# Kernel tuning notes

Hardware: AMD Instinct MI355X
Metric: run time of the kernel (lower is better)

The kernel has to match this reference:

```python
import jax, jax.numpy as jnp
import numpy as np

B, NQ, NK, D_IN, HD = 1, 16384, 7933, 1024, 512
R = 0.3  # keep-top-r fraction used for the quantile threshold


def _l2norm(x):
    # matches F.normalize(p=2, dim=-1, eps=1e-12)
    n = jnp.linalg.norm(x, axis=-1, keepdims=True)
    return x / jnp.maximum(n, 1e-12)


def setup_inputs() -> dict:
    key = jax.random.key(0)
    ks = jax.random.split(key, 10)
    s = 0.02
    return {
        "query": jax.random.normal(ks[0], (B, NQ, D_IN), jnp.float32),
        "key_x": jax.random.normal(ks[1], (B, NK, D_IN), jnp.float32),
        "wq_w": jax.random.normal(ks[2], (HD, D_IN), jnp.float32) * s,
        "wq_b": jnp.zeros((HD,), jnp.float32),
        "wk_w": jax.random.normal(ks[3], (HD, D_IN), jnp.float32) * s,
        "wk_b": jnp.zeros((HD,), jnp.float32),
        "wa_w": jax.random.normal(ks[4], (1, NK), jnp.float32) * s,
        "wa_b": jnp.zeros((1,), jnp.float32),
        "cls_w": jax.random.normal(ks[5], (1, HD), jnp.float32) * s,
        "cls_b": jnp.zeros((1,), jnp.float32),
    }


def reference(query, key_x, wq_w, wq_b, wk_w, wk_b, wa_w, wa_b, cls_w, cls_b):
    # WQ / WK: Linear + Tanh
    q = jnp.tanh(jnp.einsum("bnd,hd->bnh", query, wq_w) + wq_b)   # [B,NQ,HD]
    k = jnp.tanh(jnp.einsum("bnd,hd->bnh", key_x, wk_w) + wk_b)   # [B,NK,HD]
    # normalized dot-product scores
    A = jnp.einsum("bqh,bkh->bqk", _l2norm(q), _l2norm(k))        # [B,NQ,NK]
    # WA: Linear(NK -> 1)
    A1 = jnp.einsum("bqk,ok->bqo", A, wa_w) + wa_b                # [B,NQ,1]
    # quantile threshold from batch 0 (torch: sorted ascending, index -int(r*NQ))
    thre = jax.lax.stop_gradient(jnp.sort(A1[0, :, 0])[-int(R * NQ)])
    A1 = jnp.where(A1 > thre, A1, 0.0)                            # F.threshold(., thre, 0)
    attn = jax.nn.softmax(A1, axis=1)                             # softmax over NQ (zeros included)
    attn_t = jnp.transpose(attn, (0, 2, 1))                       # [B,1,NQ]
    z = jnp.matmul(attn_t, q).reshape(-1, HD)                     # [B,HD]
    y_prob = z @ cls_w.T + cls_b                                  # [B,1]
    return (y_prob, attn_t)
```

## Files before the change

### kernel.cpp

```cpp
#include <hip/hip_runtime.h>
#include <math.h>

#define NQ 16384
#define NK 7933
#define DI 1024
#define HD 512
#define RANK_TARGET 11469

typedef __bf16 bf16x8 __attribute__((ext_vector_type(8)));
typedef float  f32x4  __attribute__((ext_vector_type(4)));

#define GLOAD_LDS16(g, l)                                                     \
  __builtin_amdgcn_global_load_lds(                                           \
      (const __attribute__((address_space(1))) void*)(g),                     \
      (__attribute__((address_space(3))) void*)(l), 16, 0, 0)

__device__ __forceinline__ unsigned mapf(float f) {
  unsigned b = __float_as_uint(f);
  return (b & 0x80000000u) ? ~b : (b | 0x80000000u);
}

__global__ void conv_all(const float* __restrict__ q, const float* __restrict__ k,
                         const float* __restrict__ wq, const float* __restrict__ wk,
                         __bf16* __restrict__ qbf, __bf16* __restrict__ kbf,
                         __bf16* __restrict__ wqbf, __bf16* __restrict__ wkbf,
                         unsigned* __restrict__ zero_region) {
  if (blockIdx.x == 0) {
    for (int j = threadIdx.x; j < 1088; j += 256) zero_region[j] = 0u;
  }
  const int NQ8 = NQ * DI / 8;
  const int NK8 = NK * DI / 8;
  const int W8  = HD * DI / 8;
  const int total = NQ8 + NK8 + 2 * W8;
  int i = blockIdx.x * blockDim.x + threadIdx.x;
  int stride = gridDim.x * blockDim.x;
  for (; i < total; i += stride) {
    const float* s; __bf16* d; int j;
    if (i < NQ8)                 { s = q;  d = qbf;  j = i; }
    else if (i < NQ8 + NK8)      { s = k;  d = kbf;  j = i - NQ8; }
    else if (i < NQ8 + NK8 + W8) { s = wq; d = wqbf; j = i - NQ8 - NK8; }
    else                         { s = wk; d = wkbf; j = i - NQ8 - NK8 - W8; }
    float4 a = ((const float4*)s)[2 * j];
    float4 b = ((const float4*)s)[2 * j + 1];
    bf16x8 o;
    o[0] = (__bf16)a.x; o[1] = (__bf16)a.y; o[2] = (__bf16)a.z; o[3] = (__bf16)a.w;
    o[4] = (__bf16)b.x; o[5] = (__bf16)b.y; o[6] = (__bf16)b.z; o[7] = (__bf16)b.w;
    ((bf16x8*)d)[j] = o;
  }
}

template <bool FUSE_A1>
__global__ __launch_bounds__(256, 3)
void gemm_bt_tanh(const __bf16* __restrict__ A, const __bf16* __restrict__ B,
                  const float* __restrict__ bias, float* __restrict__ C, int M,
                  const float* __restrict__ v, float* __restrict__ A1dot,
                  float* __restrict__ A1ss) {
  constexpr int K = DI;
  constexpr int N = HD;
  __shared__ __align__(16) __bf16 sA[128 * 64];
  __shared__ __align__(16) __bf16 sB[128 * 64];

  const int tid  = threadIdx.x;
  const int lane = tid & 63;
  const int wave = tid >> 6;
  const int wr = wave >> 1, wc = wave & 1;
  const int m0 = blockIdx.x * 128, n0 = blockIdx.y * 128;

  const int srow = lane >> 3;
  const int scol = (((lane & 7) ^ srow)) << 3;

  const int lrow = lane & 15;
  const int chi  = lane >> 4;

  f32x4 acc[4][4] = {};

  for (int kk = 0; kk < K; kk += 64) {
    __syncthreads();
#pragma unroll
    for (int c = 0; c < 4; ++c) {
      int seg = wave * 4 + c;
      int row = seg * 8 + srow;
      int ga = m0 + row; if (ga > M - 1) ga = M - 1;
      GLOAD_LDS16(A + (size_t)ga * K + kk + scol, &sA[seg * 512]);
      GLOAD_LDS16(B + (size_t)(n0 + row) * K + kk + scol, &sB[seg * 512]);
    }
    __syncthreads();
#pragma unroll
    for (int ks = 0; ks < 64; ks += 32) {
      const int cc = (ks >> 3) + chi;
      const int sw = ((cc ^ (lrow & 7)) << 3);
      bf16x8 af[4], bfr[4];
#pragma unroll
      for (int mi = 0; mi < 4; ++mi)
        af[mi] = *(const bf16x8*)(&sA[(wr * 64 + mi * 16 + lrow) * 64 + sw]);
#pragma unroll
      for (int ni = 0; ni < 4; ++ni)
        bfr[ni] = *(const bf16x8*)(&sB[(wc * 64 + ni * 16 + lrow) * 64 + sw]);
#pragma unroll
      for (int mi = 0; mi < 4; ++mi)
#pragma unroll
        for (int ni = 0; ni < 4; ++ni)
          acc[mi][ni] = __builtin_amdgcn_mfma_f32_16x16x32_bf16(af[mi], bfr[ni], acc[mi][ni], 0, 0, 0);
    }
  }

  const int rbase = m0 + wr * 64 + ((lane >> 4) << 2);
  const int cbase = n0 + wc * 64 + (lane & 15);
  float b4[4], v4[4];
#pragma unroll
  for (int ni = 0; ni < 4; ++ni) {
    b4[ni] = bias[cbase + ni * 16];
    if constexpr (FUSE_A1) v4[ni] = v[cbase + ni * 16];
  }
#pragma unroll
  for (int mi = 0; mi < 4; ++mi) {
#pragma unroll
    for (int r = 0; r < 4; ++r) {
      int grow = rbase + mi * 16 + r;
      if (grow < M) {
        float pd = 0.f, pss = 0.f;
#pragma unroll
        for (int ni = 0; ni < 4; ++ni) {
          float val = tanhf(acc[mi][ni][r] + b4[ni]);
          C[(size_t)grow * N + cbase + ni * 16] = val;
          if constexpr (FUSE_A1) { pd += val * v4[ni]; pss += val * val; }
        }
        if constexpr (FUSE_A1) {
#pragma unroll
          for (int off = 1; off < 16; off <<= 1) {
            pd += __shfl_xor(pd, off);
            pss += __shfl_xor(pss, off);
          }
          if ((lane & 15) == 0) {
            atomicAdd(&A1dot[grow], pd);
            atomicAdd(&A1ss[grow], pss);
          }
        }
      }
    }
  }
}

__global__ __launch_bounds__(256)
void reduce_v_zero(const float* __restrict__ kt, const float* __restrict__ wa,
                   float* __restrict__ v, int M, uint2* __restrict__ zr) {
  {
    int g = blockIdx.x * 256 + threadIdx.x;
    uint2 zz; zz.x = 0u; zz.y = 0u;
    zr[g] = zz;
    if (g < 24576 - 16384) zr[16384 + g] = zz;
  }
  __shared__ float vpart[4][512];
  const int tid = threadIdx.x, lane = tid & 63, wave = tid >> 6;
  const int gw = blockIdx.x * 4 + wave;
  const int tw = gridDim.x * 4;
  float acc[8] = {0, 0, 0, 0, 0, 0, 0, 0};
  for (int r = gw; r < M; r += tw) {
    const float4* p = (const float4*)(kt + (size_t)r * HD + lane * 8);
    float4 x = p[0], y = p[1];
    float ss = x.x * x.x + x.y * x.y + x.z * x.z + x.w * x.w
             + y.x * y.x + y.y * y.y + y.z * y.z + y.w * y.w;
#pragma unroll
    for (int off = 32; off; off >>= 1) ss += __shfl_xor(ss, off);
    float s = wa[r] / fmaxf(sqrtf(ss), 1e-12f);
    acc[0] += s * x.x; acc[1] += s * x.y; acc[2] += s * x.z; acc[3] += s * x.w;
    acc[4] += s * y.x; acc[5] += s * y.y; acc[6] += s * y.z; acc[7] += s * y.w;
  }
#pragma unroll
  for (int j = 0; j < 8; ++j) vpart[wave][lane * 8 + j] = acc[j];
  __syncthreads();
  for (int c = tid; c < 512; c += 256)
    atomicAdd(&v[c], vpart[0][c] + vpart[1][c] + vpart[2][c] + vpart[3][c]);
}

__global__ __launch_bounds__(1024)
void select_kernel(const float* __restrict__ A1dot, const float* __restrict__ A1ss,
                   const float* __restrict__ wa_b, float* __restrict__ A1,
                   unsigned* __restrict__ keyg, float* __restrict__ scf) {
  __shared__ unsigned wred1[16], wred2[16], wred3[16];
  __shared__ unsigned s_res;
  const int t = threadIdx.x, lane = t & 63, wave = t >> 6;
  const float wab = wa_b[0];
  unsigned kloc[16];
#pragma unroll 4
  for (int j = 0; j < 16; ++j) {
    int i = j * 1024 + t;
    float d = A1dot[i], ss = A1ss[i];
    float a1 = d / fmaxf(sqrtf(ss), 1e-12f) + wab;
    A1[i] = a1;
    unsigned k = mapf(a1);
    kloc[j] = k;
    keyg[i] = k;
  }
  if (t == 0) s_res = 0u;
  __syncthreads();

  for (int b = 30; b >= 0; b -= 2) {
    const unsigned res = s_res;
    const unsigned t1 = res | (1u << b);
    const unsigned t2 = res | (2u << b);
    const unsigned t3 = res | (3u << b);
    unsigned c1 = 0, c2 = 0, c3 = 0;
#pragma unroll
    for (int j = 0; j < 16; ++j) {
      unsigned k = kloc[j];
      c1 += (k < t1); c2 += (k < t2); c3 += (k < t3);
    }
#pragma unroll
    for (int off = 32; off; off >>= 1) {
      c1 += __shfl_xor(c1, off);
      c2 += __shfl_xor(c2, off);
      c3 += __shfl_xor(c3, off);
    }
    if (lane == 0) { wred1[wave] = c1; wred2[wave] = c2; wred3[wave] = c3; }
    __syncthreads();
    if (t == 0) {
      unsigned C1 = 0, C2 = 0, C3 = 0;
      for (int w = 0; w < 16; ++w) { C1 += wred1[w]; C2 += wred2[w]; C3 += wred3[w]; }
      unsigned nr = res;
      if (C3 <= RANK_TARGET)      nr = t3;
      else if (C2 <= RANK_TARGET) nr = t2;
      else if (C1 <= RANK_TARGET) nr = t1;
      s_res = nr;
    }
    __syncthreads();
  }
  if (t == 0) {
    unsigned key = s_res;
    unsigned bits = (key & 0x80000000u) ? (key ^ 0x80000000u) : ~key;
    scf[0] = __uint_as_float(bits);
  }
}

__global__ __launch_bounds__(256)
void expz(const float* __restrict__ A1, const float* __restrict__ qt,
          float* __restrict__ scf, float* __restrict__ e_out,
          float* __restrict__ z) {
  __shared__ float vpart[4][512];
  __shared__ float esum[4];
  const int tid = threadIdx.x, lane = tid & 63, wave = tid >> 6;
  const float thre = scf[0];
  const int gw = blockIdx.x * 4 + wave;
  const int tw = gridDim.x * 4;
  float acc[8] = {0, 0, 0, 0, 0, 0, 0, 0};
  float es = 0.f;
  for (int r = gw; r < NQ; r += tw) {
    float x = A1[r]; x = (x > thre) ? x : 0.f;
    float e = expf(x - thre);
    if (lane == 0) e_out[r] = e;
    es += e;
    const float4* p = (const float4*)(qt + (size_t)r * HD + lane * 8);
    float4 u = p[0], w = p[1];
    acc[0] += e * u.x; acc[1] += e * u.y; acc[2] += e * u.z; acc[3] += e * u.w;
    acc[4] += e * w.x; acc[5] += e * w.y; acc[6] += e * w.z; acc[7] += e * w.w;
  }
  if (lane == 0) esum[wave] = es;
#pragma unroll
  for (int j = 0; j < 8; ++j) vpart[wave][lane * 8 + j] = acc[j];
  __syncthreads();
  for (int c = tid; c < 512; c += 256)
    atomicAdd(&z[c], vpart[0][c] + vpart[1][c] + vpart[2][c] + vpart[3][c]);
  if (tid == 0) atomicAdd(&scf[2], esum[0] + esum[1] + esum[2] + esum[3]);
}

__global__ __launch_bounds__(256)
void finalize(float* __restrict__ attn, const float* __restrict__ scf,
              const float* __restrict__ z, const float* __restrict__ cls_w,
              const float* __restrict__ cls_b, float* __restrict__ y) {
  const float invZ = 1.f / scf[2];
  if (blockIdx.x < 64) {
    int i = blockIdx.x * 256 + threadIdx.x;
    attn[i] *= invZ;
  } else if (threadIdx.x < 64) {
    const int lane = threadIdx.x;
    const float4* zp = (const float4*)(z + lane * 8);
    const float4* wp = (const float4*)(cls_w + lane * 8);
    float4 a = zp[0], b = zp[1], c = wp[0], d = wp[1];
    float dot = a.x * c.x + a.y * c.y + a.z * c.z + a.w * c.w
              + b.x * d.x + b.y * d.y + b.z * d.z + b.w * d.w;
#pragma unroll
    for (int off = 32; off; off >>= 1) dot += __shfl_xor(dot, off);
    if (lane == 0) y[0] = dot * invZ + cls_b[0];
  }
}

#define OFF_WQBF 0u
#define OFF_WKBF 1048576u
#define OFF_A1D  1048576u
#define OFF_A1S  1114112u
#define OFF_KEY  1179648u
#define OFF_QBF  2097152u
#define OFF_A1   35651584u
#define OFF_V    35717120u
#define OFF_Z    35719168u
#define OFF_SC   35721216u
#define OFF_KBF  35721472u
#define OFF_KT   51968256u
#define OFF_QT   35721472u

extern "C" void kernel_launch(void* const* d_in, const int* in_sizes, int n_in,
                              void* d_out, int out_size, void* d_ws, size_t ws_size,
                              hipStream_t stream) {
  const float* query = (const float*)d_in[0];
  const float* key_x = (const float*)d_in[1];
  const float* wq_w  = (const float*)d_in[2];
  const float* wq_b  = (const float*)d_in[3];
  const float* wk_w  = (const float*)d_in[4];
  const float* wk_b  = (const float*)d_in[5];
  const float* wa_w  = (const float*)d_in[6];
  const float* wa_b  = (const float*)d_in[7];
  const float* cls_w = (const float*)d_in[8];
  const float* cls_b = (const float*)d_in[9];
  float* out = (float*)d_out;

  char* ws = (char*)d_ws;
  __bf16* wqbf  = (__bf16*)(ws + OFF_WQBF);
  __bf16* wkbf  = (__bf16*)(ws + OFF_WKBF);
  float*  A1dot = (float*)(ws + OFF_A1D);
  float*  A1ss  = (float*)(ws + OFF_A1S);
  unsigned* keyg = (unsigned*)(ws + OFF_KEY);
  __bf16* qbf   = (__bf16*)(ws + OFF_QBF);
  float*  A1    = (float*)(ws + OFF_A1);
  float*  v     = (float*)(ws + OFF_V);
  float*  z     = (float*)(ws + OFF_Z);
  float*  scf   = (float*)(ws + OFF_SC);
  __bf16* kbf   = (__bf16*)(ws + OFF_KBF);
  float*  ktanh = (float*)(ws + OFF_KT);
  float*  qtanh = (float*)(ws + OFF_QT);
  float*  out_attn = out + 1;

  conv_all<<<4096, 256, 0, stream>>>(query, key_x, wq_w, wk_w,
                                     qbf, kbf, wqbf, wkbf, (unsigned*)v);

  gemm_bt_tanh<false><<<dim3(62, 4), 256, 0, stream>>>(
      kbf, wkbf, wk_b, ktanh, NK, nullptr, nullptr, nullptr);

  reduce_v_zero<<<64, 256, 0, stream>>>(ktanh, wa_w, v, NK, (uint2*)A1dot);

  gemm_bt_tanh<true><<<dim3(128, 4), 256, 0, stream>>>(
      qbf, wqbf, wq_b, qtanh, NQ, v, A1dot, A1ss);

  select_kernel<<<1, 1024, 0, stream>>>(A1dot, A1ss, wa_b, A1, keyg, scf);

  expz<<<128, 256, 0, stream>>>(A1, qtanh, scf, out_attn, z);

  finalize<<<65, 256, 0, stream>>>(out_attn, scf, z, cls_w, cls_b, out);
}
```

Measured before the change: 280.8 us.

## Fold softmax sum into select, fuse finalize into expz via last-block reduction

The softmax denominator is now computed inside the single-block select kernel from register-held keys, so expz can write normalized attention directly. The classifier dot product moves into the last block of expz, detected with an atomic counter, which removes the finalize launch and the extra pass over attention. The global key buffer write and part of the zeroing are dropped. The GEMM launch-bounds occupancy hint also changes from 3 to 2 blocks per SM, and the select kernel gains an extra serial exp pass.

```diff
diff --git a/kernel.cpp b/kernel.cpp
--- a/kernel.cpp
+++ b/kernel.cpp
@@ -18,6 +18,10 @@
 __device__ __forceinline__ unsigned mapf(float f) {
   unsigned b = __float_as_uint(f);
   return (b & 0x80000000u) ? ~b : (b | 0x80000000u);
+}
+__device__ __forceinline__ float unmapf(unsigned key) {
+  unsigned bits = (key & 0x80000000u) ? (key ^ 0x80000000u) : ~key;
+  return __uint_as_float(bits);
 }
 
 __global__ void conv_all(const float* __restrict__ q, const float* __restrict__ k,
@@ -50,7 +54,7 @@
 }
 
 template <bool FUSE_A1>
-__global__ __launch_bounds__(256, 3)
+__global__ __launch_bounds__(256, 2)
 void gemm_bt_tanh(const __bf16* __restrict__ A, const __bf16* __restrict__ B,
                   const float* __restrict__ bias, float* __restrict__ C, int M,
                   const float* __restrict__ v, float* __restrict__ A1dot,
@@ -148,7 +152,6 @@
     int g = blockIdx.x * 256 + threadIdx.x;
     uint2 zz; zz.x = 0u; zz.y = 0u;
     zr[g] = zz;
-    if (g < 24576 - 16384) zr[16384 + g] = zz;
   }
   __shared__ float vpart[4][512];
   const int tid = threadIdx.x, lane = tid & 63, wave = tid >> 6;
@@ -176,8 +179,9 @@
 __global__ __launch_bounds__(1024)
 void select_kernel(const float* __restrict__ A1dot, const float* __restrict__ A1ss,
                    const float* __restrict__ wa_b, float* __restrict__ A1,
-                   unsigned* __restrict__ keyg, float* __restrict__ scf) {
+                   float* __restrict__ scf) {
   __shared__ unsigned wred1[16], wred2[16], wred3[16];
+  __shared__ float fred[16];
   __shared__ unsigned s_res;
   const int t = threadIdx.x, lane = t & 63, wave = t >> 6;
   const float wab = wa_b[0];
@@ -188,9 +192,7 @@
     float d = A1dot[i], ss = A1ss[i];
     float a1 = d / fmaxf(sqrtf(ss), 1e-12f) + wab;
     A1[i] = a1;
-    unsigned k = mapf(a1);
-    kloc[j] = k;
-    keyg[i] = k;
+    kloc[j] = mapf(a1);
   }
   if (t == 0) s_res = 0u;
   __syncthreads();
@@ -225,62 +227,72 @@
     }
     __syncthreads();
   }
+  const float thre = unmapf(s_res);
+  float es = 0.f;
+#pragma unroll
+  for (int j = 0; j < 16; ++j) {
+    float x = unmapf(kloc[j]);
+    x = (x > thre) ? x : 0.f;
+    es += expf(x - thre);
+  }
+#pragma unroll
+  for (int off = 32; off; off >>= 1) es += __shfl_xor(es, off);
+  if (lane == 0) fred[wave] = es;
+  __syncthreads();
   if (t == 0) {
-    unsigned key = s_res;
-    unsigned bits = (key & 0x80000000u) ? (key ^ 0x80000000u) : ~key;
-    scf[0] = __uint_as_float(bits);
+    float S = 0.f;
+    for (int w = 0; w < 16; ++w) S += fred[w];
+    scf[0] = thre;
+    scf[2] = S;
   }
 }
 
 __global__ __launch_bounds__(256)
 void expz(const float* __restrict__ A1, const float* __restrict__ qt,
-          float* __restrict__ scf, float* __restrict__ e_out,
-          float* __restrict__ z) {
+          float* __restrict__ scf, float* __restrict__ out_attn,
+          float* __restrict__ z, const float* __restrict__ cls_w,
+          const float* __restrict__ cls_b, float* __restrict__ out_y) {
   __shared__ float vpart[4][512];
-  __shared__ float esum[4];
+  __shared__ int s_last;
   const int tid = threadIdx.x, lane = tid & 63, wave = tid >> 6;
-  const float thre = scf[0];
+  const float thre = scf[0], invZ = 1.f / scf[2];
   const int gw = blockIdx.x * 4 + wave;
   const int tw = gridDim.x * 4;
   float acc[8] = {0, 0, 0, 0, 0, 0, 0, 0};
-  float es = 0.f;
   for (int r = gw; r < NQ; r += tw) {
     float x = A1[r]; x = (x > thre) ? x : 0.f;
-    float e = expf(x - thre);
-    if (lane == 0) e_out[r] = e;
-    es += e;
+    float a = expf(x - thre) * invZ;
+    if (lane == 0) out_attn[r] = a;
     const float4* p = (const float4*)(qt + (size_t)r * HD + lane * 8);
     float4 u = p[0], w = p[1];
-    acc[0] += e * u.x; acc[1] += e * u.y; acc[2] += e * u.z; acc[3] += e * u.w;
-    acc[4] += e * w.x; acc[5] += e * w.y; acc[6] += e * w.z; acc[7] += e * w.w;
-  }
-  if (lane == 0) esum[wave] = es;
+    acc[0] += a * u.x; acc[1] += a * u.y; acc[2] += a * u.z; acc[3] += a * u.w;
+    acc[4] += a * w.x; acc[5] += a * w.y; acc[6] += a * w.z; acc[7] += a * w.w;
+  }
 #pragma unroll
   for (int j = 0; j < 8; ++j) vpart[wave][lane * 8 + j] = acc[j];
   __syncthreads();
   for (int c = tid; c < 512; c += 256)
     atomicAdd(&z[c], vpart[0][c] + vpart[1][c] + vpart[2][c] + vpart[3][c]);
-  if (tid == 0) atomicAdd(&scf[2], esum[0] + esum[1] + esum[2] + esum[3]);
-}
-
-__global__ __launch_bounds__(256)
-void finalize(float* __restrict__ attn, const float* __restrict__ scf,
-              const float* __restrict__ z, const float* __restrict__ cls_w,
-              const float* __restrict__ cls_b, float* __restrict__ y) {
-  const float invZ = 1.f / scf[2];
-  if (blockIdx.x < 64) {
-    int i = blockIdx.x * 256 + threadIdx.x;
-    attn[i] *= invZ;
-  } else if (threadIdx.x < 64) {
-    const int lane = threadIdx.x;
-    const float4* zp = (const float4*)(z + lane * 8);
-    const float4* wp = (const float4*)(cls_w + lane * 8);
-    float4 a = zp[0], b = zp[1], c = wp[0], d = wp[1];
-    float dot = a.x * c.x + a.y * c.y + a.z * c.z + a.w * c.w
-              + b.x * d.x + b.y * d.y + b.z * d.z + b.w * d.w;
+
+  __syncthreads();
+  if (tid == 0) {
+    __threadfence();
+    unsigned prev = __hip_atomic_fetch_add((unsigned*)&scf[3], 1u,
+                                           __ATOMIC_ACQ_REL, __HIP_MEMORY_SCOPE_AGENT);
+    s_last = (prev == (unsigned)(gridDim.x - 1));
+  }
+  __syncthreads();
+  if (s_last && wave == 0) {
+    float dot = 0.f;
+#pragma unroll
+    for (int j = 0; j < 8; ++j) {
+      float zz = __hip_atomic_load(&z[lane * 8 + j], __ATOMIC_RELAXED,
+                                   __HIP_MEMORY_SCOPE_AGENT);
+      dot += zz * cls_w[lane * 8 + j];
+    }
 #pragma unroll
     for (int off = 32; off; off >>= 1) dot += __shfl_xor(dot, off);
-    if (lane == 0) y[0] = dot * invZ + cls_b[0];
+    if (lane == 0) out_y[0] = dot + cls_b[0];
   }
 }
 
@@ -288,7 +300,6 @@
 #define OFF_WKBF 1048576u
 #define OFF_A1D  1048576u
 #define OFF_A1S  1114112u
-#define OFF_KEY  1179648u
 #define OFF_QBF  2097152u
 #define OFF_A1   35651584u
 #define OFF_V    35717120u
@@ -318,7 +329,6 @@
   __bf16* wkbf  = (__bf16*)(ws + OFF_WKBF);
   float*  A1dot = (float*)(ws + OFF_A1D);
   float*  A1ss  = (float*)(ws + OFF_A1S);
-  unsigned* keyg = (unsigned*)(ws + OFF_KEY);
   __bf16* qbf   = (__bf16*)(ws + OFF_QBF);
   float*  A1    = (float*)(ws + OFF_A1);
   float*  v     = (float*)(ws + OFF_V);
@@ -340,9 +350,7 @@
   gemm_bt_tanh<true><<<dim3(128, 4), 256, 0, stream>>>(
       qbf, wqbf, wq_b, qtanh, NQ, v, A1dot, A1ss);
 
-  select_kernel<<<1, 1024, 0, stream>>>(A1dot, A1ss, wa_b, A1, keyg, scf);
-
-  expz<<<128, 256, 0, stream>>>(A1, qtanh, scf, out_attn, z);
-
-  finalize<<<65, 256, 0, stream>>>(out_attn, scf, z, cls_w, cls_b, out);
-}
+  select_kernel<<<1, 1024, 0, stream>>>(A1dot, A1ss, wa_b, A1, scf);
+
+  expz<<<128, 256, 0, stream>>>(A1, qtanh, scf, out_attn, z, cls_w, cls_b, out);
+}
```

After: 284.4 us. Within noise of the previous version (+1.3%).
